# Kernel tuning notes

Hardware: AMD Instinct MI355X
Metric: run time of the kernel (lower is better)

The kernel has to match this reference:

```python
import jax, jax.numpy as jnp
import numpy as np

B, D_IN, EXPERT_DIM, N_EXPERT, N_TASK = 16384, 1024, 256, 8, 4


def setup_inputs() -> dict:
    key = jax.random.key(0)
    k1, k2, k3 = jax.random.split(key, 3)
    x = jax.random.normal(k1, (B, D_IN), dtype=jnp.float32)
    # Glorot-ish scaling for weights
    We = jax.random.normal(k2, (N_EXPERT, D_IN, EXPERT_DIM), dtype=jnp.float32) * (1.0 / np.sqrt(D_IN))
    be = jnp.zeros((N_EXPERT, EXPERT_DIM), dtype=jnp.float32)
    Wg = jax.random.normal(k3, (N_TASK, D_IN, N_EXPERT), dtype=jnp.float32) * (1.0 / np.sqrt(D_IN))
    bg = jnp.zeros((N_TASK, N_EXPERT), dtype=jnp.float32)
    return {"x": x, "We": We, "be": be, "Wg": Wg, "bg": bg}


def reference(x, We, be, Wg, bg):
    # Experts: grouped GEMM -> [B, n_expert, expert_dim]
    E = jax.nn.relu(jnp.einsum("bd,edh->beh", x, We) + be[None, :, :])
    # Gates: [B, n_task, n_expert], softmax over experts
    G = jax.nn.softmax(jnp.einsum("bd,tde->bte", x, Wg) + bg[None, :, :], axis=-1)
    # Gated combine per task: towers[t] = E^T @ g_t -> [n_task, B, expert_dim]
    towers = jnp.einsum("beh,bte->tbh", E, G)
    return towers  # stacked version of the original list of [B, expert_dim] towers
```

## Files before the change

### kernel.cpp

```cpp
#include <hip/hip_runtime.h>

#define B_ROWS 16384
#define D_IN   1024
#define H_DIM  256
#define N_EXP  8
#define N_TASK 4
#define NKT    16

typedef short bf16x8 __attribute__((ext_vector_type(8)));
typedef float f32x4  __attribute__((ext_vector_type(4)));
typedef unsigned short u16x8 __attribute__((ext_vector_type(8)));

static __device__ __forceinline__ unsigned short f2bf(float f) {
  unsigned int u = __float_as_uint(f);
  u += 0x7fffu + ((u >> 16) & 1u);
  return (unsigned short)(u >> 16);
}

#define WS_XB   0u
#define WS_WET  33554432u
#define WS_WGT  37748736u
#define WS_GT   37814272u

__global__ void k_prep_w(const float* __restrict__ x, const float* __restrict__ We,
                         const float* __restrict__ Wg,
                         unsigned short* __restrict__ x_b,
                         unsigned short* __restrict__ We_t, unsigned short* __restrict__ Wg_t) {
  int bid = blockIdx.x;
  int t = threadIdx.x;
  if (bid < 512) {
    int e = bid >> 6;
    int tl = bid & 63;
    int k0 = (tl >> 2) * 64, h0 = (tl & 3) * 64;
    __shared__ unsigned short tile[64][72];
    const float* src = We + (size_t)e * (D_IN * H_DIM);
#pragma unroll
    for (int i = 0; i < 4; ++i) {
      int kk = (t >> 4) + i * 16;
      int hh = (t & 15) * 4;
      float4 v = *(const float4*)(src + (size_t)(k0 + kk) * H_DIM + h0 + hh);
      tile[hh + 0][kk] = f2bf(v.x);
      tile[hh + 1][kk] = f2bf(v.y);
      tile[hh + 2][kk] = f2bf(v.z);
      tile[hh + 3][kk] = f2bf(v.w);
    }
    __syncthreads();
    unsigned short* dst = We_t + (size_t)e * (H_DIM * D_IN);
#pragma unroll
    for (int i = 0; i < 4; ++i) {
      int hh = (t >> 4) + i * 16;
      int kk = (t & 15) * 4;
      ushort4 u = *(const ushort4*)&tile[hh][kk];
      *(ushort4*)(dst + (size_t)(h0 + hh) * D_IN + k0 + kk) = u;
    }
  } else if (bid < 544) {
    int n = bid - 512;
    int tsk = n >> 3, e = n & 7;
    int k = t * 4;
    const float* src = Wg + (size_t)tsk * (D_IN * 8) + e;
    ushort4 u;
    u.x = f2bf(src[(size_t)(k + 0) * 8]);
    u.y = f2bf(src[(size_t)(k + 1) * 8]);
    u.z = f2bf(src[(size_t)(k + 2) * 8]);
    u.w = f2bf(src[(size_t)(k + 3) * 8]);
    *(ushort4*)(Wg_t + (size_t)n * D_IN + k) = u;
  } else {
    size_t base = (size_t)(bid - 544) * 2048 + (size_t)t * 8;
    float4 v0 = *(const float4*)(x + base);
    float4 v1 = *(const float4*)(x + base + 4);
    u16x8 u;
    u[0] = (short)f2bf(v0.x); u[1] = (short)f2bf(v0.y);
    u[2] = (short)f2bf(v0.z); u[3] = (short)f2bf(v0.w);
    u[4] = (short)f2bf(v1.x); u[5] = (short)f2bf(v1.y);
    u[6] = (short)f2bf(v1.z); u[7] = (short)f2bf(v1.w);
    *(u16x8*)(x_b + base) = u;
  }
}

__global__ void k_gates(const unsigned short* __restrict__ x_b,
                        const unsigned short* __restrict__ Wg_t,
                        const float* __restrict__ bg,
                        float* __restrict__ Gt) {
  __shared__ unsigned short xs[64][136];
  __shared__ unsigned short wgs[32][136];
  int m0 = blockIdx.x * 64;
  int t = threadIdx.x;
  int wv = t >> 6, l = t & 63;
  f32x4 acc0 = {0.f, 0.f, 0.f, 0.f}, acc1 = {0.f, 0.f, 0.f, 0.f};

  for (int k0 = 0; k0 < D_IN; k0 += 128) {
    {
      int r = t >> 2;
      int cb = (t & 3) * 32;
      const unsigned short* p = x_b + (size_t)(m0 + r) * D_IN + k0 + cb;
#pragma unroll
      for (int i = 0; i < 4; ++i)
        *(u16x8*)&xs[r][cb + i * 8] = *(const u16x8*)(p + i * 8);
    }
    {
      int n = t >> 3;
      int kk = (t & 7) * 16;
      const unsigned short* p = Wg_t + (size_t)n * D_IN + k0 + kk;
#pragma unroll
      for (int i = 0; i < 4; ++i)
        *(ushort4*)&wgs[n][kk + i * 4] = *(const ushort4*)(p + i * 4);
    }
    __syncthreads();
#pragma unroll
    for (int kk = 0; kk < 4; ++kk) {
      bf16x8 a  = *(const bf16x8*)&xs[wv * 16 + (l & 15)][kk * 32 + (l >> 4) * 8];
      bf16x8 b0 = *(const bf16x8*)&wgs[(l & 15)][kk * 32 + (l >> 4) * 8];
      bf16x8 b1 = *(const bf16x8*)&wgs[16 + (l & 15)][kk * 32 + (l >> 4) * 8];
      acc0 = __builtin_amdgcn_mfma_f32_16x16x32_bf16(a, b0, acc0, 0, 0, 0);
      acc1 = __builtin_amdgcn_mfma_f32_16x16x32_bf16(a, b1, acc1, 0, 0, 0);
    }
    __syncthreads();
  }

  int colb = l & 15;
  int rbase = m0 + wv * 16 + (l >> 4) * 4;
  float bga = bg[colb], bgb = bg[16 + colb];
#pragma unroll
  for (int j = 0; j < 4; ++j) {
    float va = acc0[j] + bga;
    float vb = acc1[j] + bgb;
    float mxa = va, mxb = vb;
#pragma unroll
    for (int d = 1; d < 8; d <<= 1) {
      mxa = fmaxf(mxa, __shfl_xor(mxa, d));
      mxb = fmaxf(mxb, __shfl_xor(mxb, d));
    }
    va = __expf(va - mxa); vb = __expf(vb - mxb);
    float sa = va, sb = vb;
#pragma unroll
    for (int d = 1; d < 8; d <<= 1) {
      sa += __shfl_xor(sa, d);
      sb += __shfl_xor(sb, d);
    }
    va /= sa; vb /= sb;
    Gt[(size_t)colb * B_ROWS + rbase + j]        = va;
    Gt[(size_t)(16 + colb) * B_ROWS + rbase + j] = vb;
  }
}

__global__ __launch_bounds__(512, 2) void k_expert(const unsigned short* __restrict__ x_b,
                                                   const unsigned short* __restrict__ We_t,
                                                   const float* __restrict__ be,
                                                   const float* __restrict__ Gt,
                                                   float* __restrict__ out) {
  __shared__ unsigned short As[2][256 * 64];
  __shared__ unsigned short Bs[2][256 * 64];
  int bid = blockIdx.x;
  int t = threadIdx.x;

  int xcd = bid & 7;
  int idx = bid >> 3;
  int m   = xcd * 8 + (idx >> 3);
  int hs  = idx & 7;
  int m0  = m * 256;

  int w  = t >> 6, l = t & 63;
  int wm = w >> 2, wn = w & 3;
  int lr = l & 15, lq = l >> 4;

  const unsigned short* Ab = x_b + (size_t)m0 * D_IN;

  const int sr = t >> 3, sg = t & 7;
  const int swz0 = ((lq ^ (lr & 7)) << 3);
  const int swz1 = (((4 + lq) ^ (lr & 7)) << 3);
  const int arow0 = (wm * 128 + lr) << 6;
  const int brow0 = (wn * 64 + lr) << 6;

  size_t bsrc[4];
#pragma unroll
  for (int q2 = 0; q2 < 4; ++q2) {
    int rq = q2 * 64 + sr;
    int me = (rq >> 3) & 7;
    int mh = hs * 32 + ((rq >> 6) & 3) * 8 + (rq & 7);
    bsrc[q2] = (size_t)(me * H_DIM + mh) * D_IN + (size_t)((sg ^ (rq & 7)) << 3);
  }

  f32x4 acc[8][4];
#pragma unroll
  for (int i = 0; i < 8; ++i)
#pragma unroll
    for (int j = 0; j < 4; ++j) acc[i][j] = (f32x4){0.f, 0.f, 0.f, 0.f};

#define STAGE_A(cb, kt, h)                                                                       \
  do {                                                                                           \
    int r0_ = (h) * 128 + sr;                                                                    \
    int r1_ = r0_ + 64;                                                                          \
    __builtin_amdgcn_global_load_lds(                                                            \
        (const __attribute__((address_space(1))) void*)(Ab + (size_t)r0_ * D_IN + (kt) * 64 +    \
                                                        ((sg ^ (r0_ & 7)) << 3)),                \
        (__attribute__((address_space(3))) void*)(&As[(cb)][r0_ * 64 + sg * 8]), 16, 0, 0);      \
    __builtin_amdgcn_global_load_lds(                                                            \
        (const __attribute__((address_space(1))) void*)(Ab + (size_t)r1_ * D_IN + (kt) * 64 +    \
                                                        ((sg ^ (r1_ & 7)) << 3)),                \
        (__attribute__((address_space(3))) void*)(&As[(cb)][r1_ * 64 + sg * 8]), 16, 0, 0);      \
  } while (0)
#define STAGE_B(cb, kt, h)                                                                       \
  do {                                                                                           \
    int r0_ = (h) * 128 + sr;                                                                    \
    int r1_ = r0_ + 64;                                                                          \
    __builtin_amdgcn_global_load_lds(                                                            \
        (const __attribute__((address_space(1))) void*)(We_t + bsrc[2 * (h)] + (kt) * 64),       \
        (__attribute__((address_space(3))) void*)(&Bs[(cb)][r0_ * 64 + sg * 8]), 16, 0, 0);      \
    __builtin_amdgcn_global_load_lds(                                                            \
        (const __attribute__((address_space(1))) void*)(We_t + bsrc[2 * (h) + 1] + (kt) * 64),   \
        (__attribute__((address_space(3))) void*)(&Bs[(cb)][r1_ * 64 + sg * 8]), 16, 0, 0);      \
  } while (0)

  STAGE_A(0, 0, 0); STAGE_A(0, 0, 1);
  STAGE_B(0, 0, 0); STAGE_B(0, 0, 1);
  STAGE_B(1, 1, 0); STAGE_B(1, 1, 1);
  asm volatile("s_waitcnt vmcnt(4)" ::: "memory");
  __builtin_amdgcn_s_barrier();

#pragma unroll 2
  for (int kt = 0; kt < NKT; ++kt) {
    int c = kt & 1;
    const unsigned short* Ap = &As[c][0];
    const unsigned short* Bp = &Bs[c][0];
    bf16x8 b0[4], b1[4];
#pragma unroll
    for (int q = 0; q < 4; ++q) {
      if (q == 0) {
#pragma unroll
        for (int fn = 0; fn < 4; ++fn) {
          b0[fn] = *(const bf16x8*)(Bp + brow0 + fn * 1024 + swz0);
          b1[fn] = *(const bf16x8*)(Bp + brow0 + fn * 1024 + swz1);
        }
      }
      bf16x8 a00 = *(const bf16x8*)(Ap + arow0 + (2 * q) * 1024 + swz0);
      bf16x8 a01 = *(const bf16x8*)(Ap + arow0 + (2 * q) * 1024 + swz1);
      bf16x8 a10 = *(const bf16x8*)(Ap + arow0 + (2 * q + 1) * 1024 + swz0);
      bf16x8 a11 = *(const bf16x8*)(Ap + arow0 + (2 * q + 1) * 1024 + swz1);
      if (q == 0)      { if (kt + 1 < NKT) STAGE_A(c ^ 1, kt + 1, 0); }
      else if (q == 1) { if (kt + 1 < NKT) STAGE_A(c ^ 1, kt + 1, 1); }
      else if (q == 2) { if (kt + 2 < NKT) STAGE_B(c, kt + 2, 0); }
      else             { if (kt + 2 < NKT) STAGE_B(c, kt + 2, 1); }
      __builtin_amdgcn_s_barrier();
      asm volatile("s_waitcnt lgkmcnt(0)" ::: "memory");
      __builtin_amdgcn_s_setprio(1);
#pragma unroll
      for (int fn = 0; fn < 4; ++fn) {
        acc[2 * q][fn]     = __builtin_amdgcn_mfma_f32_16x16x32_bf16(a00, b0[fn], acc[2 * q][fn], 0, 0, 0);
        acc[2 * q][fn]     = __builtin_amdgcn_mfma_f32_16x16x32_bf16(a01, b1[fn], acc[2 * q][fn], 0, 0, 0);
        acc[2 * q + 1][fn] = __builtin_amdgcn_mfma_f32_16x16x32_bf16(a10, b0[fn], acc[2 * q + 1][fn], 0, 0, 0);
        acc[2 * q + 1][fn] = __builtin_amdgcn_mfma_f32_16x16x32_bf16(a11, b1[fn], acc[2 * q + 1][fn], 0, 0, 0);
      }
      __builtin_amdgcn_s_setprio(0);
      if (q == 3) {
        if (kt < NKT - 2)        asm volatile("s_waitcnt vmcnt(4)" ::: "memory");
        else if (kt == NKT - 2)  asm volatile("s_waitcnt vmcnt(0)" ::: "memory");
      }
      __builtin_amdgcn_s_barrier();
    }
  }
#undef STAGE_A
#undef STAGE_B

  int hi = lr >> 3, h7 = lr & 7;
  int hglob = hs * 32 + wn * 8 + h7;
  float bev[4];
#pragma unroll
  for (int fn = 0; fn < 4; ++fn)
    bev[fn] = be[(2 * fn + hi) * H_DIM + hglob];
#pragma unroll
  for (int fm = 0; fm < 8; ++fm) {
    int r0 = m0 + wm * 128 + fm * 16 + lq * 4;
    float vv[4][4];
#pragma unroll
    for (int fn = 0; fn < 4; ++fn)
#pragma unroll
      for (int j = 0; j < 4; ++j)
        vv[fn][j] = fmaxf(acc[fm][fn][j] + bev[fn], 0.f);
#pragma unroll
    for (int tk = 0; tk < 4; ++tk) {
      float4 gv[4];
#pragma unroll
      for (int fn = 0; fn < 4; ++fn)
        gv[fn] = *(const float4*)(Gt + (size_t)(tk * 8 + 2 * fn + hi) * B_ROWS + r0);
      float s0 = gv[0].x * vv[0][0] + gv[1].x * vv[1][0] + gv[2].x * vv[2][0] + gv[3].x * vv[3][0];
      float s1 = gv[0].y * vv[0][1] + gv[1].y * vv[1][1] + gv[2].y * vv[2][1] + gv[3].y * vv[3][1];
      float s2 = gv[0].z * vv[0][2] + gv[1].z * vv[1][2] + gv[2].z * vv[2][2] + gv[3].z * vv[3][2];
      float s3 = gv[0].w * vv[0][3] + gv[1].w * vv[1][3] + gv[2].w * vv[2][3] + gv[3].w * vv[3][3];
      s0 += __shfl_xor(s0, 8);
      s1 += __shfl_xor(s1, 8);
      s2 += __shfl_xor(s2, 8);
      s3 += __shfl_xor(s3, 8);
      if ((tk >> 1) == hi) {
        float* o = out + ((size_t)tk * B_ROWS + r0) * H_DIM + hglob;
        o[0]                 = s0;
        o[(size_t)H_DIM]     = s1;
        o[(size_t)H_DIM * 2] = s2;
        o[(size_t)H_DIM * 3] = s3;
      }
    }
  }
}

extern "C" void kernel_launch(void* const* d_in, const int* in_sizes, int n_in,
                              void* d_out, int out_size, void* d_ws, size_t ws_size,
                              hipStream_t stream) {
  const float* x  = (const float*)d_in[0];
  const float* We = (const float*)d_in[1];
  const float* be = (const float*)d_in[2];
  const float* Wg = (const float*)d_in[3];
  const float* bg = (const float*)d_in[4];
  float* out = (float*)d_out;
  char* ws = (char*)d_ws;
  unsigned short* x_b  = (unsigned short*)(ws + WS_XB);
  unsigned short* We_t = (unsigned short*)(ws + WS_WET);
  unsigned short* Wg_t = (unsigned short*)(ws + WS_WGT);
  float*          Gt   = (float*)(ws + WS_GT);

  k_prep_w<<<544 + 8192, 256, 0, stream>>>(x, We, Wg, x_b, We_t, Wg_t);
  k_gates<<<B_ROWS / 64, 256, 0, stream>>>(x_b, Wg_t, bg, Gt);
  k_expert<<<512, 512, 0, stream>>>(x_b, We_t, be, Gt, out);
}
```

Before: 208.1 us.

## Fuse x bf16 conversion into gate kernel and halve combine shuffles

The fp32-to-bf16 conversion of x moves out of the prep kernel and into the gate GEMM. The gate kernel now reads fp32 x directly, converts it in registers, writes x_b for the expert kernel, and feeds MFMA straight from registers. It split-K's across 4 waves with an LDS reduction, which removes one full pass over x_b. The expert epilogue also computes all four task partials first, then pairs them so only two shuffles per row are needed instead of four wasted-half shuffles. The cost is a gate kernel with more blocks that does redundant Wg loads per block without LDS staging.

Measured after the change: 209.3 us. Within noise of the previous version (+0.6%).

```diff
diff --git a/kernel.cpp b/kernel.cpp
--- a/kernel.cpp
+++ b/kernel.cpp
@@ -22,9 +22,7 @@
 #define WS_WGT  37748736u
 #define WS_GT   37814272u
 
-__global__ void k_prep_w(const float* __restrict__ x, const float* __restrict__ We,
-                         const float* __restrict__ Wg,
-                         unsigned short* __restrict__ x_b,
+__global__ void k_prep_w(const float* __restrict__ We, const float* __restrict__ Wg,
                          unsigned short* __restrict__ We_t, unsigned short* __restrict__ Wg_t) {
   int bid = blockIdx.x;
   int t = threadIdx.x;
@@ -53,7 +51,7 @@
       ushort4 u = *(const ushort4*)&tile[hh][kk];
       *(ushort4*)(dst + (size_t)(h0 + hh) * D_IN + k0 + kk) = u;
     }
-  } else if (bid < 544) {
+  } else {
     int n = bid - 512;
     int tsk = n >> 3, e = n & 7;
     int k = t * 4;
@@ -64,82 +62,81 @@
     u.z = f2bf(src[(size_t)(k + 2) * 8]);
     u.w = f2bf(src[(size_t)(k + 3) * 8]);
     *(ushort4*)(Wg_t + (size_t)n * D_IN + k) = u;
-  } else {
-    size_t base = (size_t)(bid - 544) * 2048 + (size_t)t * 8;
-    float4 v0 = *(const float4*)(x + base);
-    float4 v1 = *(const float4*)(x + base + 4);
-    u16x8 u;
-    u[0] = (short)f2bf(v0.x); u[1] = (short)f2bf(v0.y);
-    u[2] = (short)f2bf(v0.z); u[3] = (short)f2bf(v0.w);
-    u[4] = (short)f2bf(v1.x); u[5] = (short)f2bf(v1.y);
-    u[6] = (short)f2bf(v1.z); u[7] = (short)f2bf(v1.w);
-    *(u16x8*)(x_b + base) = u;
-  }
-}
-
-__global__ void k_gates(const unsigned short* __restrict__ x_b,
-                        const unsigned short* __restrict__ Wg_t,
-                        const float* __restrict__ bg,
-                        float* __restrict__ Gt) {
-  __shared__ unsigned short xs[64][136];
-  __shared__ unsigned short wgs[32][136];
-  int m0 = blockIdx.x * 64;
+  }
+}
+
+__global__ __launch_bounds__(256) void k_gates(const float* __restrict__ x,
+                                               const unsigned short* __restrict__ Wg_t,
+                                               unsigned short* __restrict__ x_b,
+                                               const float* __restrict__ bg,
+                                               float* __restrict__ Gt) {
+  __shared__ float red[4][16][36];
+  int m0 = blockIdx.x * 16;
   int t = threadIdx.x;
-  int wv = t >> 6, l = t & 63;
+  int w = t >> 6, l = t & 63;
+  int lr = l & 15, lq = l >> 4;
+  int kbase = w * 256;
   f32x4 acc0 = {0.f, 0.f, 0.f, 0.f}, acc1 = {0.f, 0.f, 0.f, 0.f};
 
-  for (int k0 = 0; k0 < D_IN; k0 += 128) {
-    {
-      int r = t >> 2;
-      int cb = (t & 3) * 32;
-      const unsigned short* p = x_b + (size_t)(m0 + r) * D_IN + k0 + cb;
-#pragma unroll
-      for (int i = 0; i < 4; ++i)
-        *(u16x8*)&xs[r][cb + i * 8] = *(const u16x8*)(p + i * 8);
-    }
-    {
-      int n = t >> 3;
-      int kk = (t & 7) * 16;
-      const unsigned short* p = Wg_t + (size_t)n * D_IN + k0 + kk;
-#pragma unroll
-      for (int i = 0; i < 4; ++i)
-        *(ushort4*)&wgs[n][kk + i * 4] = *(const ushort4*)(p + i * 4);
-    }
-    __syncthreads();
-#pragma unroll
-    for (int kk = 0; kk < 4; ++kk) {
-      bf16x8 a  = *(const bf16x8*)&xs[wv * 16 + (l & 15)][kk * 32 + (l >> 4) * 8];
-      bf16x8 b0 = *(const bf16x8*)&wgs[(l & 15)][kk * 32 + (l >> 4) * 8];
-      bf16x8 b1 = *(const bf16x8*)&wgs[16 + (l & 15)][kk * 32 + (l >> 4) * 8];
-      acc0 = __builtin_amdgcn_mfma_f32_16x16x32_bf16(a, b0, acc0, 0, 0, 0);
-      acc1 = __builtin_amdgcn_mfma_f32_16x16x32_bf16(a, b1, acc1, 0, 0, 0);
-    }
-    __syncthreads();
-  }
-
-  int colb = l & 15;
-  int rbase = m0 + wv * 16 + (l >> 4) * 4;
-  float bga = bg[colb], bgb = bg[16 + colb];
+  const float* xrow = x + (size_t)(m0 + lr) * D_IN;
+  unsigned short* xbrow = x_b + (size_t)(m0 + lr) * D_IN;
+  const unsigned short* wg0 = Wg_t + (size_t)lr * D_IN;
+  const unsigned short* wg1 = Wg_t + (size_t)(16 + lr) * D_IN;
+
+#pragma unroll
+  for (int ks = 0; ks < 8; ++ks) {
+    int k = kbase + ks * 32 + lq * 8;
+    float4 v0 = *(const float4*)(xrow + k);
+    float4 v1 = *(const float4*)(xrow + k + 4);
+    bf16x8 a;
+    a[0] = (short)f2bf(v0.x); a[1] = (short)f2bf(v0.y);
+    a[2] = (short)f2bf(v0.z); a[3] = (short)f2bf(v0.w);
+    a[4] = (short)f2bf(v1.x); a[5] = (short)f2bf(v1.y);
+    a[6] = (short)f2bf(v1.z); a[7] = (short)f2bf(v1.w);
+    *(bf16x8*)(xbrow + k) = a;
+    bf16x8 b0 = *(const bf16x8*)(wg0 + k);
+    bf16x8 b1 = *(const bf16x8*)(wg1 + k);
+    acc0 = __builtin_amdgcn_mfma_f32_16x16x32_bf16(a, b0, acc0, 0, 0, 0);
+    acc1 = __builtin_amdgcn_mfma_f32_16x16x32_bf16(a, b1, acc1, 0, 0, 0);
+  }
+
 #pragma unroll
   for (int j = 0; j < 4; ++j) {
-    float va = acc0[j] + bga;
-    float vb = acc1[j] + bgb;
-    float mxa = va, mxb = vb;
-#pragma unroll
-    for (int d = 1; d < 8; d <<= 1) {
-      mxa = fmaxf(mxa, __shfl_xor(mxa, d));
-      mxb = fmaxf(mxb, __shfl_xor(mxb, d));
-    }
-    va = __expf(va - mxa); vb = __expf(vb - mxb);
-    float sa = va, sb = vb;
-#pragma unroll
-    for (int d = 1; d < 8; d <<= 1) {
-      sa += __shfl_xor(sa, d);
-      sb += __shfl_xor(sb, d);
-    }
-    va /= sa; vb /= sb;
-    Gt[(size_t)colb * B_ROWS + rbase + j]        = va;
-    Gt[(size_t)(16 + colb) * B_ROWS + rbase + j] = vb;
+    red[w][lq * 4 + j][lr]      = acc0[j];
+    red[w][lq * 4 + j][16 + lr] = acc1[j];
+  }
+  __syncthreads();
+  if (w == 0) {
+#pragma unroll
+    for (int j = 0; j < 4; ++j) {
+      int rr = lq * 4 + j;
+      acc0[j] = red[0][rr][lr] + red[1][rr][lr] + red[2][rr][lr] + red[3][rr][lr];
+      acc1[j] = red[0][rr][16 + lr] + red[1][rr][16 + lr] + red[2][rr][16 + lr] + red[3][rr][16 + lr];
+    }
+    int colb = lr;
+    int rbase = m0 + lq * 4;
+    float bga = bg[colb], bgb = bg[16 + colb];
+#pragma unroll
+    for (int j = 0; j < 4; ++j) {
+      float va = acc0[j] + bga;
+      float vb = acc1[j] + bgb;
+      float mxa = va, mxb = vb;
+#pragma unroll
+      for (int d = 1; d < 8; d <<= 1) {
+        mxa = fmaxf(mxa, __shfl_xor(mxa, d));
+        mxb = fmaxf(mxb, __shfl_xor(mxb, d));
+      }
+      va = __expf(va - mxa); vb = __expf(vb - mxb);
+      float sa = va, sb = vb;
+#pragma unroll
+      for (int d = 1; d < 8; d <<= 1) {
+        sa += __shfl_xor(sa, d);
+        sb += __shfl_xor(sb, d);
+      }
+      va /= sa; vb /= sb;
+      Gt[(size_t)colb * B_ROWS + rbase + j]        = va;
+      Gt[(size_t)(16 + colb) * B_ROWS + rbase + j] = vb;
+    }
   }
 }
 
@@ -276,27 +273,29 @@
 #pragma unroll
       for (int j = 0; j < 4; ++j)
         vv[fn][j] = fmaxf(acc[fm][fn][j] + bev[fn], 0.f);
+    float p[4][4];
 #pragma unroll
     for (int tk = 0; tk < 4; ++tk) {
-      float4 gv[4];
+      f32x4 gv[4];
 #pragma unroll
       for (int fn = 0; fn < 4; ++fn)
-        gv[fn] = *(const float4*)(Gt + (size_t)(tk * 8 + 2 * fn + hi) * B_ROWS + r0);
-      float s0 = gv[0].x * vv[0][0] + gv[1].x * vv[1][0] + gv[2].x * vv[2][0] + gv[3].x * vv[3][0];
-      float s1 = gv[0].y * vv[0][1] + gv[1].y * vv[1][1] + gv[2].y * vv[2][1] + gv[3].y * vv[3][1];
-      float s2 = gv[0].z * vv[0][2] + gv[1].z * vv[1][2] + gv[2].z * vv[2][2] + gv[3].z * vv[3][2];
-      float s3 = gv[0].w * vv[0][3] + gv[1].w * vv[1][3] + gv[2].w * vv[2][3] + gv[3].w * vv[3][3];
-      s0 += __shfl_xor(s0, 8);
-      s1 += __shfl_xor(s1, 8);
-      s2 += __shfl_xor(s2, 8);
-      s3 += __shfl_xor(s3, 8);
-      if ((tk >> 1) == hi) {
-        float* o = out + ((size_t)tk * B_ROWS + r0) * H_DIM + hglob;
-        o[0]                 = s0;
-        o[(size_t)H_DIM]     = s1;
-        o[(size_t)H_DIM * 2] = s2;
-        o[(size_t)H_DIM * 3] = s3;
-      }
+        gv[fn] = *(const f32x4*)(Gt + (size_t)(tk * 8 + 2 * fn + hi) * B_ROWS + r0);
+#pragma unroll
+      for (int j = 0; j < 4; ++j)
+        p[tk][j] = gv[0][j] * vv[0][j] + gv[1][j] * vv[1][j] +
+                   gv[2][j] * vv[2][j] + gv[3][j] * vv[3][j];
+    }
+#pragma unroll
+    for (int j = 0; j < 4; ++j) {
+      float sa = hi ? p[0][j] : p[2][j];
+      float sb = hi ? p[1][j] : p[3][j];
+      float ra = __shfl_xor(sa, 8);
+      float rb = __shfl_xor(sb, 8);
+      float t0 = (hi ? p[2][j] : p[0][j]) + ra;
+      float t1 = (hi ? p[3][j] : p[1][j]) + rb;
+      size_t tk0 = (size_t)(hi * 2);
+      out[(tk0 * B_ROWS + r0 + j) * H_DIM + hglob]       = t0;
+      out[((tk0 + 1) * B_ROWS + r0 + j) * H_DIM + hglob] = t1;
     }
   }
 }
@@ -316,7 +315,7 @@
   unsigned short* Wg_t = (unsigned short*)(ws + WS_WGT);
   float*          Gt   = (float*)(ws + WS_GT);
 
-  k_prep_w<<<544 + 8192, 256, 0, stream>>>(x, We, Wg, x_b, We_t, Wg_t);
-  k_gates<<<B_ROWS / 64, 256, 0, stream>>>(x_b, Wg_t, bg, Gt);
+  k_prep_w<<<544, 256, 0, stream>>>(We, Wg, We_t, Wg_t);
+  k_gates<<<B_ROWS / 16, 256, 0, stream>>>(x, Wg_t, x_b, bg, Gt);
   k_expert<<<512, 512, 0, stream>>>(x_b, We_t, be, Gt, out);
 }
```
